# Performance work log

Measured on AMD Instinct MI355X. Metric: run time of the kernel, lower is better.

Reference implementation:

```python
import jax, jax.numpy as jnp
import numpy as np

T = 2048          # num tokens
HID = 2048        # hidden size
H = 16            # num heads
DN = 128          # qk_nope_head_dim
DR = 64           # qk_rope_head_dim
DV = 128          # v_head_dim
KV = 512          # kv_lora_rank
EPS = 1e-6
THETA = 10000.0
SCALE = (DN + DR) ** -0.5


def rmsnorm(x, w):
    var = jnp.mean(x * x, axis=-1, keepdims=True)
    return x * jax.lax.rsqrt(var + EPS) * w


def rope_interleaved(x, cos, sin):
    # x: [..., DR]; cos/sin broadcastable to [..., DR//2]; non-neox (interleaved pairs)
    x1 = x[..., 0::2]
    x2 = x[..., 1::2]
    o1 = x1 * cos - x2 * sin
    o2 = x2 * cos + x1 * sin
    return jnp.stack([o1, o2], axis=-1).reshape(x.shape)


def setup_inputs() -> dict:
    key = jax.random.key(0)
    ks = jax.random.split(key, 6)
    s = lambda fan_in: 1.0 / np.sqrt(fan_in)
    return {
        "positions": jnp.arange(T, dtype=jnp.int32),
        "hidden_states": jax.random.normal(ks[0], (T, HID), dtype=jnp.float32),
        "w_q": jax.random.normal(ks[1], (HID, H * (DN + DR)), dtype=jnp.float32) * s(HID),
        "w_kv_a": jax.random.normal(ks[2], (HID, KV + DR), dtype=jnp.float32) * s(HID),
        "kv_a_ln_w": jnp.ones((KV,), dtype=jnp.float32),
        "w_kv_b": jax.random.normal(ks[3], (KV, H * (DN + DV)), dtype=jnp.float32) * s(KV),
        "w_o": jax.random.normal(ks[4], (H * DV, HID), dtype=jnp.float32) * s(H * DV),
    }


def reference(positions, hidden_states, w_q, w_kv_a, kv_a_ln_w, w_kv_b, w_o):
    # Q projection (q_lora_rank is None -> direct q_proj)
    q = (hidden_states @ w_q).reshape(T, H, DN + DR)
    q_nope, q_pe = q[..., :DN], q[..., DN:]

    # KV latent + decoupled rope key
    kv = hidden_states @ w_kv_a              # [T, KV+DR]
    kv_c = rmsnorm(kv[:, :KV], kv_a_ln_w)    # [T, KV]
    k_pe = kv[:, KV:]                        # [T, DR]

    # RoPE (non-neox / interleaved)
    inv_freq = 1.0 / (THETA ** (jnp.arange(0, DR, 2, dtype=jnp.float32) / DR))
    freqs = positions.astype(jnp.float32)[:, None] * inv_freq   # [T, DR//2]
    cos, sin = jnp.cos(freqs), jnp.sin(freqs)
    q_pe = rope_interleaved(q_pe, cos[:, None, :], sin[:, None, :])  # [T, H, DR]
    k_pe = rope_interleaved(k_pe, cos, sin)                          # [T, DR]

    # Up-project latent to per-head K_nope / V
    kvb = (kv_c @ w_kv_b).reshape(T, H, DN + DV)
    k_nope, v = kvb[..., :DN], kvb[..., DN:]

    qf = jnp.concatenate([q_nope, q_pe], axis=-1)                    # [T, H, DN+DR]
    kf = jnp.concatenate([k_nope, jnp.broadcast_to(k_pe[:, None, :], (T, H, DR))], axis=-1)

    scores = jnp.einsum("qhd,khd->hqk", qf, kf) * SCALE              # [H, T, T]
    causal = jnp.tril(jnp.ones((T, T), dtype=bool))
    scores = jnp.where(causal, scores, jnp.finfo(scores.dtype).min)
    attn = jax.nn.softmax(scores, axis=-1)

    out = jnp.einsum("hqk,khd->qhd", attn, v).reshape(T, H * DV)
    return out @ w_o                                                 # [T, HID]
```

## Files before the change

kernel.cpp:

```cpp
#include <hip/hip_runtime.h>
#include <hip/hip_bf16.h>
#include <stdint.h>

#define T_N  2048
#define HID  2048
#define NH   16
#define DN   128
#define DR   64
#define DV   128
#define KVD  512
#define DQK  192
#define QDIM 3072
#define KVBD 4096
#define KVA  576
#define QKVN 3712
#define QBLK 128
#define KVBLK 64
#define TPH  40

typedef short  s16x8 __attribute__((ext_vector_type(8)));
typedef float  f32x4 __attribute__((ext_vector_type(4)));
typedef unsigned short u16;
typedef unsigned short u16x2 __attribute__((ext_vector_type(2)));
typedef unsigned short u16x4 __attribute__((ext_vector_type(4)));

#define NEG_INF (-__builtin_inff())
#define AS1 __attribute__((address_space(1)))
#define AS3 __attribute__((address_space(3)))
__device__ __constant__ float SCALE_C = 0.07216878364870323f;

__device__ __forceinline__ u16 f2b(float f) {
  unsigned u = __float_as_uint(f);
  u += 0x7fffu + ((u >> 16) & 1u);
  return (u16)(u >> 16);
}
__device__ __forceinline__ float b2f(u16 v) {
  return __uint_as_float(((unsigned)v) << 16);
}

__global__ void cast_and_tab(const float* __restrict__ x, u16* __restrict__ y,
                             const int* __restrict__ pos, float* __restrict__ ctab,
                             float* __restrict__ stab) {
  const int bid = blockIdx.x, tid = threadIdx.x;
  if (bid < 4096) {
    int i = bid * 256 + tid;
    float4 v = ((const float4*)x)[i];
    u16x4 o;
    o.x = f2b(v.x); o.y = f2b(v.y); o.z = f2b(v.z); o.w = f2b(v.w);
    ((u16x4*)y)[i] = o;
  } else {
    int i = (bid - 4096) * 256 + tid;
    int t = i >> 5, j = i & 31;
    float inv = powf(10000.f, -(float)(2 * j) / 64.f);
    float f = (float)pos[t] * inv;
    float s, c;
    sincosf(f, &s, &c);
    ctab[i] = c; stab[i] = s;
  }
}

#define TQK (QKVN / 32)
#define NB0 (TQK * (HID / 32))
#define NB1 ((KVBD / 32) * (KVD / 32))
#define NB2 ((HID / 32) * ((NH * DV) / 32))
__global__ void prep_weights(const float* __restrict__ wq, const float* __restrict__ wkva,
                             const float* __restrict__ wkvb, const float* __restrict__ wo,
                             u16* __restrict__ wqkvT, u16* __restrict__ wkvbT,
                             u16* __restrict__ woT)
{
  __shared__ float tile[32][33];
  int bid = blockIdx.x;
  const int tx = threadIdx.x, ty = threadIdx.y;
  int reg, n0, k0, K, N;
  const float* src = nullptr;
  u16* dst;
  if (bid < NB0)            { reg = 0; n0 = (bid % TQK) * 32;         k0 = (bid / TQK) * 32;         K = HID;     N = QKVN; dst = wqkvT; }
  else if (bid < NB0 + NB1) { bid -= NB0; reg = 1; n0 = (bid % (KVBD/32)) * 32; k0 = (bid / (KVBD/32)) * 32; K = KVD;  N = KVBD; src = wkvb; dst = wkvbT; }
  else                      { bid -= NB0 + NB1; reg = 2; n0 = (bid % (HID/32)) * 32; k0 = (bid / (HID/32)) * 32; K = NH*DV; N = HID; src = wo; dst = woT; }
#pragma unroll
  for (int i = 0; i < 4; ++i) {
    const int n = n0 + tx, k = k0 + ty + i * 8;
    float val;
    if (reg == 0) {
      if (n < QDIM) val = wq[(size_t)k * QDIM + n];
      else { int n2 = n - QDIM; val = (n2 < KVA) ? wkva[(size_t)k * KVA + n2] : 0.f; }
    } else {
      val = src[(size_t)k * N + n];
    }
    tile[ty + i * 8][tx] = val;
  }
  __syncthreads();
#pragma unroll
  for (int i = 0; i < 4; ++i)
    dst[(size_t)(n0 + ty + i * 8) * K + k0 + tx] = f2b(tile[tx][ty + i * 8]);
}

template <int MODE>
__global__ __launch_bounds__(256) void gemm_bf16(
    const u16* __restrict__ A, const u16* __restrict__ Bt,
    void* __restrict__ Cout, u16* __restrict__ vT, int M, int N, int K)
{
  __shared__ __align__(16) u16 As[8192];
  __shared__ __align__(16) u16 Bs[8192];
  const int tid  = threadIdx.x;
  const int lane = tid & 63;
  const int w    = tid >> 6;

  const int nwg = gridDim.x * gridDim.y;
  int id = blockIdx.y * gridDim.x + blockIdx.x;
  id = (id & 7) * (nwg >> 3) + (id >> 3);
  const int m0 = (id / gridDim.x) * 128, n0 = (id % gridDim.x) * 128;

  const int wm = (w >> 1) * 64, wn = (w & 1) * 64;

  const int r0   = tid >> 3;
  const int selE = (((tid & 7) ^ (r0 & 7)) << 3);
  const u16* sA = A  + (size_t)(m0 + r0) * K + selE;
  const u16* sB = Bt + (size_t)(n0 + r0) * K + selE;
  const int ldsOff = tid * 8;

  f32x4 acc[4][4];
  const f32x4 zero = {0.f, 0.f, 0.f, 0.f};
#pragma unroll
  for (int m = 0; m < 4; ++m)
#pragma unroll
    for (int n = 0; n < 4; ++n) acc[m][n] = zero;

  const int arow = lane & 15;
  const int kb   = (lane >> 4) * 16;
  const int KT = K >> 6;

  for (int kt = 0; kt < KT; ++kt) {
    const int ko = kt << 6;
    __syncthreads();
#pragma unroll
    for (int j = 0; j < 4; ++j) {
      __builtin_amdgcn_global_load_lds((const AS1 unsigned*)(sA + ko + (size_t)j * 32 * K),
                                       (AS3 unsigned*)(&As[ldsOff + j * 2048]), 16, 0, 0);
      __builtin_amdgcn_global_load_lds((const AS1 unsigned*)(sB + ko + (size_t)j * 32 * K),
                                       (AS3 unsigned*)(&Bs[ldsOff + j * 2048]), 16, 0, 0);
    }
    __syncthreads();
#pragma unroll
    for (int kk = 0; kk < 2; ++kk) {
      s16x8 af[4], bfr[4];
#pragma unroll
      for (int m = 0; m < 4; ++m) {
        const int r = wm + m * 16 + arow;
        af[m] = *(const s16x8*)((const char*)As + r * 128 + ((kk * 64 + kb) ^ ((r & 7) << 4)));
      }
#pragma unroll
      for (int n = 0; n < 4; ++n) {
        const int r = wn + n * 16 + arow;
        bfr[n] = *(const s16x8*)((const char*)Bs + r * 128 + ((kk * 64 + kb) ^ ((r & 7) << 4)));
      }
#pragma unroll
      for (int m = 0; m < 4; ++m)
#pragma unroll
        for (int n = 0; n < 4; ++n)
          acc[m][n] = __builtin_amdgcn_mfma_f32_16x16x32_bf16(af[m], bfr[n], acc[m][n], 0, 0, 0);
    }
  }

  const int r0w = (lane >> 4) * 4;
  const int cc = lane & 15;
  if constexpr (MODE == 2) {
    const int h = n0 >> 8;
    const bool vhalf = (n0 >> 7) & 1;
    u16* kf = (u16*)Cout;
#pragma unroll
    for (int m = 0; m < 4; ++m)
#pragma unroll
      for (int n = 0; n < 4; ++n) {
        const int d = wn + n * 16 + cc;
        const int trow = m0 + wm + m * 16 + r0w;
        if (!vhalf) {
#pragma unroll
          for (int r = 0; r < 4; ++r)
            kf[(size_t)(trow + r) * QDIM + h * DQK + d] = f2b(acc[m][n][r]);
        } else {
          u16x4 o;
          o.x = f2b(acc[m][n][0]); o.y = f2b(acc[m][n][1]);
          o.z = f2b(acc[m][n][2]); o.w = f2b(acc[m][n][3]);
          *(u16x4*)&vT[((size_t)h * 128 + d) * T_N + trow] = o;
        }
      }
  } else {
#pragma unroll
    for (int m = 0; m < 4; ++m)
#pragma unroll
      for (int n = 0; n < 4; ++n)
#pragma unroll
        for (int r = 0; r < 4; ++r) {
          const size_t idx = (size_t)(m0 + wm + m * 16 + r0w + r) * N + (n0 + wn + n * 16 + cc);
          if constexpr (MODE == 1) ((u16*)Cout)[idx] = f2b(acc[m][n][r]);
          else                     ((float*)Cout)[idx] = acc[m][n][r];
        }
  }
}

__global__ __launch_bounds__(256) void post_qkva(
    const u16* __restrict__ qkv, const float* __restrict__ lnw,
    const float* __restrict__ ctab, const float* __restrict__ stab,
    u16* __restrict__ kvc, u16* __restrict__ kf, u16* __restrict__ qfo)
{
  const int t = blockIdx.x;
  const int tid = threadIdx.x;
  __shared__ float csh[32], ssh[32], wsum[4];
  __shared__ u16 kpesh[64];
  if (tid < 32) { csh[tid] = ctab[t * 32 + tid]; ssh[tid] = stab[t * 32 + tid]; }

  const u16* row = qkv + (size_t)t * QKVN + QDIM;
  u16x2 v2 = *(const u16x2*)(row + tid * 2);
  float vx = b2f(v2.x), vy = b2f(v2.y);
  float ss = vx * vx + vy * vy;
#pragma unroll
  for (int d = 1; d < 64; d <<= 1) ss += __shfl_xor(ss, d, 64);
  if ((tid & 63) == 0) wsum[tid >> 6] = ss;
  __syncthreads();
  float tot = wsum[0] + wsum[1] + wsum[2] + wsum[3];
  float rs = rsqrtf(tot * (1.f / 512.f) + 1e-6f);
  float2 wv = *(const float2*)(lnw + tid * 2);
  kvc[(size_t)t * 512 + tid * 2]     = f2b(vx * rs * wv.x);
  kvc[(size_t)t * 512 + tid * 2 + 1] = f2b(vy * rs * wv.y);
  if (tid < 32) {
    float x1 = b2f(row[512 + 2 * tid]), x2 = b2f(row[513 + 2 * tid]);
    kpesh[2 * tid]     = f2b(x1 * csh[tid] - x2 * ssh[tid]);
    kpesh[2 * tid + 1] = f2b(x2 * csh[tid] + x1 * ssh[tid]);
  }
  __syncthreads();
  {
    const int h = tid >> 4, d0 = (tid & 15) * 4;
    u16x4 kp = *(const u16x4*)&kpesh[d0];
    *(u16x4*)&kf[(size_t)t * QDIM + h * DQK + 128 + d0] = kp;
  }

  const float SC = SCALE_C;
#pragma unroll
  for (int i = 0; i < 6; ++i) {
    const int p = i * 256 + tid;
    const int h = p / 96, pr = p % 96;
    const u16* base = qkv + (size_t)t * QKVN + h * DQK;
    u16* ob = qfo + ((size_t)t * NH + h) * DQK;
    if (pr < 64) {
      int d = pr * 2;
      u16x2 v = *(const u16x2*)(base + d);
      ob[d]     = f2b(b2f(v.x) * SC);
      ob[d + 1] = f2b(b2f(v.y) * SC);
    } else {
      int j = pr - 64;
      u16x2 v = *(const u16x2*)(base + 128 + 2 * j);
      ob[128 + 2 * j]     = f2b((b2f(v.x) * csh[j] - b2f(v.y) * ssh[j]) * SC);
      ob[128 + 2 * j + 1] = f2b((b2f(v.y) * csh[j] + b2f(v.x) * ssh[j]) * SC);
    }
  }
}

__global__ __launch_bounds__(512) void attn_fwd(
    const u16* __restrict__ qf, const u16* __restrict__ kf,
    const u16* __restrict__ vT, u16* __restrict__ Opart,
    float* __restrict__ mpart, float* __restrict__ lpart)
{
  const int h = blockIdx.x;
  const int j = (TPH - 1) - blockIdx.y;
  int qt, c, S;
  if (j < 4)       { qt = j;                c = 0;        S = 1; }
  else if (j < 12) { int u = j-4;  qt = 4 + (u>>1);  c = u&1;     S = 2; }
  else if (j < 24) { int u = j-12; int q3 = u/3; qt = 8+q3; c = u-3*q3; S = 3; }
  else             { int u = j-24; qt = 12 + (u>>2); c = u&3;     S = 4; }
  const int n = 2 * qt + 2;
  const int kt0 = (c * n) / S, kt1 = ((c + 1) * n) / S;
  const int task = h * TPH + j;
  const int q0 = qt * QBLK;

  const int tid = threadIdx.x;
  const int w = tid >> 6, lane = tid & 63;
  const int qw = q0 + w * 16;
  const int l15 = lane & 15, lh = lane >> 4;
  const int qrow = qw + l15;

  __shared__ __align__(16) u16 Ks[KVBLK * 192];
  __shared__ __align__(16) u16 Vs[128 * 64];
  __shared__ __align__(16) u16 P[8][16][72];

  s16x8 aQ[6];
#pragma unroll
  for (int kg = 0; kg < 6; ++kg)
    aQ[kg] = *(const s16x8*)&qf[(size_t)qrow * QDIM + h * DQK + kg * 32 + lh * 8];

  f32x4 accO[8];
  const f32x4 zero = {0.f, 0.f, 0.f, 0.f};
#pragma unroll
  for (int vn = 0; vn < 8; ++vn) accO[vn] = zero;
  float mreg = NEG_INF, lreg = 0.f;

  const int rK = tid >> 3, cK = (tid & 7) * 16;
  const int rV = tid >> 2, cV = (tid & 3) * 16;
  const u16* gK = kf + (size_t)rK * QDIM + h * DQK;
  const u16* gV = vT + ((size_t)h * 128 + rV) * T_N;
  const int swK = (rK & 7) << 4;
  const int swV = (rV & 7) << 4;

  s16x8 stK[3], stV[2];
#pragma unroll
  for (int jj = 0; jj < 3; ++jj)
    stK[jj] = *(const s16x8*)((const char*)(gK + (size_t)(kt0 * KVBLK) * QDIM) + cK + jj * 128);
#pragma unroll
  for (int jj = 0; jj < 2; ++jj)
    stV[jj] = *(const s16x8*)((const char*)(gV + kt0 * KVBLK) + cV + jj * 64);

  for (int kt = kt0; kt < kt1; ++kt) {
    const int t0 = kt * KVBLK;
    __syncthreads();
#pragma unroll
    for (int jj = 0; jj < 3; ++jj)
      *(s16x8*)((char*)Ks + rK * 384 + ((cK + jj * 128) ^ swK)) = stK[jj];
#pragma unroll
    for (int jj = 0; jj < 2; ++jj)
      *(s16x8*)((char*)Vs + rV * 128 + ((cV + jj * 64) ^ swV)) = stV[jj];
    __syncthreads();
    if (kt + 1 < kt1) {
      const int tn = t0 + KVBLK;
#pragma unroll
      for (int jj = 0; jj < 3; ++jj)
        stK[jj] = *(const s16x8*)((const char*)(gK + (size_t)tn * QDIM) + cK + jj * 128);
#pragma unroll
      for (int jj = 0; jj < 2; ++jj)
        stV[jj] = *(const s16x8*)((const char*)(gV + tn) + cV + jj * 64);
    }

    f32x4 s[4];
#pragma unroll
    for (int ct = 0; ct < 4; ++ct) s[ct] = zero;
    const int swq = (l15 & 7) << 4;
    __builtin_amdgcn_s_setprio(1);
#pragma unroll
    for (int ct = 0; ct < 4; ++ct) {
      const char* kbase = (char*)Ks + (ct * 16 + l15) * 384;
#pragma unroll
      for (int kg = 0; kg < 6; ++kg) {
        s16x8 aK = *(const s16x8*)(kbase + ((kg * 64 + lh * 16) ^ swq));
        s[ct] = __builtin_amdgcn_mfma_f32_16x16x32_bf16(aK, aQ[kg], s[ct], 0, 0, 0);
      }
    }
    __builtin_amdgcn_s_setprio(0);

    const bool diag = (t0 + KVBLK > q0);
    if (diag) {
#pragma unroll
      for (int ct = 0; ct < 4; ++ct)
#pragma unroll
        for (int r = 0; r < 4; ++r)
          s[ct][r] = (t0 + ct * 16 + lh * 4 + r <= qrow) ? s[ct][r] : NEG_INF;
    }

    float mx = s[0][0];
#pragma unroll
    for (int ct = 0; ct < 4; ++ct)
#pragma unroll
      for (int r = 0; r < 4; ++r) mx = fmaxf(mx, s[ct][r]);
    mx = fmaxf(mx, __shfl_xor(mx, 16, 64));
    mx = fmaxf(mx, __shfl_xor(mx, 32, 64));
    if (mx > mreg + 8.f) {
      float sc = __expf(mreg - mx);
      lreg *= sc;
#pragma unroll
      for (int vn = 0; vn < 8; ++vn)
#pragma unroll
        for (int r = 0; r < 4; ++r) accO[vn][r] *= sc;
      mreg = mx;
    }
    float p[4][4];
    float ps = 0.f;
#pragma unroll
    for (int ct = 0; ct < 4; ++ct)
#pragma unroll
      for (int r = 0; r < 4; ++r) { p[ct][r] = __expf(s[ct][r] - mreg); ps += p[ct][r]; }
    ps += __shfl_xor(ps, 16, 64);
    ps += __shfl_xor(ps, 32, 64);
    lreg += ps;

#pragma unroll
    for (int ct = 0; ct < 4; ++ct) {
      u16x4 pk;
      pk.x = f2b(p[ct][0]); pk.y = f2b(p[ct][1]);
      pk.z = f2b(p[ct][2]); pk.w = f2b(p[ct][3]);
      *(u16x4*)&P[w][l15][ct * 16 + lh * 4] = pk;
    }
    asm volatile("s_waitcnt lgkmcnt(0)" ::: "memory");
    s16x8 pb0 = *(const s16x8*)&P[w][l15][lh * 8];
    s16x8 pb1 = *(const s16x8*)&P[w][l15][32 + lh * 8];

    __builtin_amdgcn_s_setprio(1);
#pragma unroll
    for (int vn = 0; vn < 8; ++vn) {
      const char* vbase = (char*)Vs + (vn * 16 + l15) * 128;
      s16x8 aV0 = *(const s16x8*)(vbase + ((lh * 16) ^ swq));
      s16x8 aV1 = *(const s16x8*)(vbase + ((64 + lh * 16) ^ swq));
      accO[vn] = __builtin_amdgcn_mfma_f32_16x16x32_bf16(aV0, pb0, accO[vn], 0, 0, 0);
      accO[vn] = __builtin_amdgcn_mfma_f32_16x16x32_bf16(aV1, pb1, accO[vn], 0, 0, 0);
    }
    __builtin_amdgcn_s_setprio(0);
  }

  u16* Ob = Opart + ((size_t)task << 14);
  const int rl = w * 16 + l15;
#pragma unroll
  for (int vn = 0; vn < 8; ++vn) {
    u16x4 o;
    o.x = f2b(accO[vn][0]); o.y = f2b(accO[vn][1]);
    o.z = f2b(accO[vn][2]); o.w = f2b(accO[vn][3]);
    *(u16x4*)&Ob[rl * 128 + vn * 16 + lh * 4] = o;
  }
  if (lane < 16) {
    mpart[task * 128 + rl] = mreg;
    lpart[task * 128 + rl] = lreg;
  }
}

__global__ __launch_bounds__(256) void attn_merge(
    const u16* __restrict__ Opart, const float* __restrict__ mpart,
    const float* __restrict__ lpart, u16* __restrict__ attno)
{
  const int h = blockIdx.x >> 4, qt = blockIdx.x & 15;
  const int S = (qt >> 2) + 1;
  int base;
  if (qt < 4) base = qt; else if (qt < 8) base = 4 + 2*(qt-4);
  else if (qt < 12) base = 12 + 3*(qt-8); else base = 24 + 4*(qt-12);
  const int task0 = h * TPH + base;
  const int tid = threadIdx.x;
  __shared__ float wn[4][128];
  if (tid < 128) {
    float mc[4], lc[4];
    float M = NEG_INF;
    for (int c = 0; c < S; ++c) {
      mc[c] = mpart[(task0 + c) * 128 + tid];
      lc[c] = lpart[(task0 + c) * 128 + tid];
      M = fmaxf(M, mc[c]);
    }
    float L = 0.f, e[4];
    for (int c = 0; c < S; ++c) { e[c] = __expf(mc[c] - M); L += lc[c] * e[c]; }
    float Li = 1.f / L;
    for (int c = 0; c < S; ++c) wn[c][tid] = e[c] * Li;
  }
  __syncthreads();
  const int q0 = qt * QBLK;
#pragma unroll 4
  for (int k = 0; k < 16; ++k) {
    int bidx = k * 1024 + tid * 4;
    int row = bidx >> 7, col = bidx & 127;
    float a0 = 0.f, a1 = 0.f, a2 = 0.f, a3 = 0.f;
    for (int c = 0; c < S; ++c) {
      u16x4 v = *(const u16x4*)&Opart[(((size_t)(task0 + c)) << 14) + bidx];
      float wgt = wn[c][row];
      a0 += wgt * b2f(v.x); a1 += wgt * b2f(v.y);
      a2 += wgt * b2f(v.z); a3 += wgt * b2f(v.w);
    }
    u16x4 o; o.x = f2b(a0); o.y = f2b(a1); o.z = f2b(a2); o.w = f2b(a3);
    *(u16x4*)&attno[(size_t)(q0 + row) * (NH * DV) + h * DV + col] = o;
  }
}

extern "C" void kernel_launch(void* const* d_in, const int* in_sizes, int n_in,
                              void* d_out, int out_size, void* d_ws, size_t ws_size,
                              hipStream_t stream)
{
  const int*   positions = (const int*)d_in[0];
  const float* hs    = (const float*)d_in[1];
  const float* w_q   = (const float*)d_in[2];
  const float* w_kva = (const float*)d_in[3];
  const float* lnw   = (const float*)d_in[4];
  const float* w_kvb = (const float*)d_in[5];
  const float* w_o   = (const float*)d_in[6];
  float* out = (float*)d_out;

  char* ws = (char*)d_ws;
  size_t off = 0;
  auto take = [&](size_t bytes) {
    char* p = ws + off;
    off += (bytes + 255) & ~(size_t)255;
    return p;
  };

  u16*   hsb  = (u16*)  take((size_t)T_N * HID * 2);
  u16*   woT  = (u16*)  take((size_t)HID * (NH * DV) * 2);
  u16*   qfb  = (u16*)  take((size_t)T_N * QDIM * 2);
  u16*   kfb  = (u16*)  take((size_t)T_N * QDIM * 2);
  u16*   vTb  = (u16*)  take((size_t)NH * 128 * T_N * 2);
  float* ctab = (float*)take((size_t)T_N * 32 * 4);
  float* stab = (float*)take((size_t)T_N * 32 * 4);

  size_t un0 = off;
  u16*   wqkvT = (u16*)  take((size_t)QKVN * HID * 2);
  u16*   wkvbT = (u16*)  take((size_t)KVBD * KVD * 2);
  u16*   kvc   = (u16*)  take((size_t)T_N * KVD * 2);
  u16*   qkvb  = (u16*)  take((size_t)T_N * KVBD * 2);
  u16*   Opart = (u16*)(ws + un0);
  float* mpart = (float*)(Opart + ((size_t)NH * TPH << 14));
  float* lpart = mpart + (size_t)NH * TPH * 128;
  u16*   attno = hsb;

  (void)positions; (void)in_sizes; (void)n_in; (void)out_size; (void)ws_size;

  cast_and_tab<<<dim3(4096 + 256), dim3(256), 0, stream>>>(hs, hsb, positions, ctab, stab);
  prep_weights<<<dim3(NB0 + NB1 + NB2), dim3(32, 8), 0, stream>>>(w_q, w_kva, w_kvb, w_o,
                                                                  wqkvT, wkvbT, woT);

  gemm_bf16<1><<<dim3(QKVN / 128, T_N / 128), dim3(256), 0, stream>>>(hsb, wqkvT, qkvb, nullptr, T_N, QKVN, HID);
  post_qkva<<<dim3(T_N), dim3(256), 0, stream>>>(qkvb, lnw, ctab, stab, kvc, kfb, qfb);

  gemm_bf16<2><<<dim3(KVBD / 128, T_N / 128), dim3(256), 0, stream>>>(kvc, wkvbT, kfb, vTb, T_N, KVBD, KVD);

  attn_fwd<<<dim3(NH, TPH), dim3(512), 0, stream>>>(qfb, kfb, vTb, Opart, mpart, lpart);
  attn_merge<<<dim3(NH * 16), dim3(256), 0, stream>>>(Opart, mpart, lpart, attno);

  gemm_bf16<0><<<dim3(HID / 128, T_N / 128), dim3(256), 0, stream>>>(attno, woT, out, nullptr, T_N, HID, HID);
}
```

Measured before the change: 208.3 us.

## Merge prep kernels and replace LDS P round-trip with ds_bpermute in attention

```diff
diff --git a/kernel.cpp b/kernel.cpp
--- a/kernel.cpp
+++ b/kernel.cpp
@@ -38,39 +38,42 @@
   return __uint_as_float(((unsigned)v) << 16);
 }
 
-__global__ void cast_and_tab(const float* __restrict__ x, u16* __restrict__ y,
-                             const int* __restrict__ pos, float* __restrict__ ctab,
-                             float* __restrict__ stab) {
-  const int bid = blockIdx.x, tid = threadIdx.x;
-  if (bid < 4096) {
+#define TQK (QKVN / 32)
+#define NBC 4096
+#define NBT 256
+#define NB0 (TQK * (HID / 32))
+#define NB1 ((KVBD / 32) * (KVD / 32))
+#define NB2 ((HID / 32) * ((NH * DV) / 32))
+__global__ __launch_bounds__(256) void prep_all(
+    const float* __restrict__ hs, u16* __restrict__ hsb,
+    const int* __restrict__ pos, float* __restrict__ ctab, float* __restrict__ stab,
+    const float* __restrict__ wq, const float* __restrict__ wkva,
+    const float* __restrict__ wkvb, const float* __restrict__ wo,
+    u16* __restrict__ wqkvT, u16* __restrict__ wkvbT, u16* __restrict__ woT)
+{
+  int bid = blockIdx.x;
+  const int tid = threadIdx.x;
+  if (bid < NBC) {
     int i = bid * 256 + tid;
-    float4 v = ((const float4*)x)[i];
+    float4 v = ((const float4*)hs)[i];
     u16x4 o;
     o.x = f2b(v.x); o.y = f2b(v.y); o.z = f2b(v.z); o.w = f2b(v.w);
-    ((u16x4*)y)[i] = o;
-  } else {
-    int i = (bid - 4096) * 256 + tid;
+    ((u16x4*)hsb)[i] = o;
+    return;
+  }
+  if (bid < NBC + NBT) {
+    int i = (bid - NBC) * 256 + tid;
     int t = i >> 5, j = i & 31;
     float inv = powf(10000.f, -(float)(2 * j) / 64.f);
     float f = (float)pos[t] * inv;
     float s, c;
     sincosf(f, &s, &c);
     ctab[i] = c; stab[i] = s;
-  }
-}
-
-#define TQK (QKVN / 32)
-#define NB0 (TQK * (HID / 32))
-#define NB1 ((KVBD / 32) * (KVD / 32))
-#define NB2 ((HID / 32) * ((NH * DV) / 32))
-__global__ void prep_weights(const float* __restrict__ wq, const float* __restrict__ wkva,
-                             const float* __restrict__ wkvb, const float* __restrict__ wo,
-                             u16* __restrict__ wqkvT, u16* __restrict__ wkvbT,
-                             u16* __restrict__ woT)
-{
+    return;
+  }
+  bid -= NBC + NBT;
   __shared__ float tile[32][33];
-  int bid = blockIdx.x;
-  const int tx = threadIdx.x, ty = threadIdx.y;
+  const int tx = tid & 31, ty = tid >> 5;
   int reg, n0, k0, K, N;
   const float* src = nullptr;
   u16* dst;
@@ -256,7 +259,7 @@
   }
 }
 
-__global__ __launch_bounds__(512) void attn_fwd(
+__global__ __launch_bounds__(512, 6) void attn_fwd(
     const u16* __restrict__ qf, const u16* __restrict__ kf,
     const u16* __restrict__ vT, u16* __restrict__ Opart,
     float* __restrict__ mpart, float* __restrict__ lpart)
@@ -278,10 +281,10 @@
   const int qw = q0 + w * 16;
   const int l15 = lane & 15, lh = lane >> 4;
   const int qrow = qw + l15;
+  (void)w;
 
   __shared__ __align__(16) u16 Ks[KVBLK * 192];
   __shared__ __align__(16) u16 Vs[128 * 64];
-  __shared__ __align__(16) u16 P[8][16][72];
 
   s16x8 aQ[6];
 #pragma unroll
@@ -309,6 +312,10 @@
   for (int jj = 0; jj < 2; ++jj)
     stV[jj] = *(const s16x8*)((const char*)(gV + kt0 * KVBLK) + cV + jj * 64);
 
+  const int a0 = (l15 + ((lh & 1) << 5)) << 2;
+  const int a1 = a0 + 64;
+  const bool hi = (lh & 2) != 0;
+
   for (int kt = kt0; kt < kt1; ++kt) {
     const int t0 = kt * KVBLK;
     __syncthreads();
@@ -380,16 +387,45 @@
     ps += __shfl_xor(ps, 32, 64);
     lreg += ps;
 
-#pragma unroll
-    for (int ct = 0; ct < 4; ++ct) {
-      u16x4 pk;
-      pk.x = f2b(p[ct][0]); pk.y = f2b(p[ct][1]);
-      pk.z = f2b(p[ct][2]); pk.w = f2b(p[ct][3]);
-      *(u16x4*)&P[w][l15][ct * 16 + lh * 4] = pk;
-    }
-    asm volatile("s_waitcnt lgkmcnt(0)" ::: "memory");
-    s16x8 pb0 = *(const s16x8*)&P[w][l15][lh * 8];
-    s16x8 pb1 = *(const s16x8*)&P[w][l15][32 + lh * 8];
+    unsigned pk00 = (unsigned)f2b(p[0][0]) | ((unsigned)f2b(p[0][1]) << 16);
+    unsigned pk01 = (unsigned)f2b(p[0][2]) | ((unsigned)f2b(p[0][3]) << 16);
+    unsigned pk10 = (unsigned)f2b(p[1][0]) | ((unsigned)f2b(p[1][1]) << 16);
+    unsigned pk11 = (unsigned)f2b(p[1][2]) | ((unsigned)f2b(p[1][3]) << 16);
+    unsigned pk20 = (unsigned)f2b(p[2][0]) | ((unsigned)f2b(p[2][1]) << 16);
+    unsigned pk21 = (unsigned)f2b(p[2][2]) | ((unsigned)f2b(p[2][3]) << 16);
+    unsigned pk30 = (unsigned)f2b(p[3][0]) | ((unsigned)f2b(p[3][1]) << 16);
+    unsigned pk31 = (unsigned)f2b(p[3][2]) | ((unsigned)f2b(p[3][3]) << 16);
+
+    union { unsigned u[4]; s16x8 v; } U0, U1;
+    {
+      unsigned ta, tb;
+      ta = (unsigned)__builtin_amdgcn_ds_bpermute(a0, (int)pk00);
+      tb = (unsigned)__builtin_amdgcn_ds_bpermute(a0, (int)pk10);
+      U0.u[0] = hi ? tb : ta;
+      ta = (unsigned)__builtin_amdgcn_ds_bpermute(a0, (int)pk01);
+      tb = (unsigned)__builtin_amdgcn_ds_bpermute(a0, (int)pk11);
+      U0.u[1] = hi ? tb : ta;
+      ta = (unsigned)__builtin_amdgcn_ds_bpermute(a1, (int)pk00);
+      tb = (unsigned)__builtin_amdgcn_ds_bpermute(a1, (int)pk10);
+      U0.u[2] = hi ? tb : ta;
+      ta = (unsigned)__builtin_amdgcn_ds_bpermute(a1, (int)pk01);
+      tb = (unsigned)__builtin_amdgcn_ds_bpermute(a1, (int)pk11);
+      U0.u[3] = hi ? tb : ta;
+      ta = (unsigned)__builtin_amdgcn_ds_bpermute(a0, (int)pk20);
+      tb = (unsigned)__builtin_amdgcn_ds_bpermute(a0, (int)pk30);
+      U1.u[0] = hi ? tb : ta;
+      ta = (unsigned)__builtin_amdgcn_ds_bpermute(a0, (int)pk21);
+      tb = (unsigned)__builtin_amdgcn_ds_bpermute(a0, (int)pk31);
+      U1.u[1] = hi ? tb : ta;
+      ta = (unsigned)__builtin_amdgcn_ds_bpermute(a1, (int)pk20);
+      tb = (unsigned)__builtin_amdgcn_ds_bpermute(a1, (int)pk30);
+      U1.u[2] = hi ? tb : ta;
+      ta = (unsigned)__builtin_amdgcn_ds_bpermute(a1, (int)pk21);
+      tb = (unsigned)__builtin_amdgcn_ds_bpermute(a1, (int)pk31);
+      U1.u[3] = hi ? tb : ta;
+    }
+    s16x8 pb0 = U0.v;
+    s16x8 pb1 = U1.v;
 
     __builtin_amdgcn_s_setprio(1);
 #pragma unroll
@@ -404,7 +440,7 @@
   }
 
   u16* Ob = Opart + ((size_t)task << 14);
-  const int rl = w * 16 + l15;
+  const int rl = (tid >> 6) * 16 + l15;
 #pragma unroll
   for (int vn = 0; vn < 8; ++vn) {
     u16x4 o;
@@ -502,9 +538,8 @@
 
   (void)positions; (void)in_sizes; (void)n_in; (void)out_size; (void)ws_size;
 
-  cast_and_tab<<<dim3(4096 + 256), dim3(256), 0, stream>>>(hs, hsb, positions, ctab, stab);
-  prep_weights<<<dim3(NB0 + NB1 + NB2), dim3(32, 8), 0, stream>>>(w_q, w_kva, w_kvb, w_o,
-                                                                  wqkvT, wkvbT, woT);
+  prep_all<<<dim3(NBC + NBT + NB0 + NB1 + NB2), dim3(256), 0, stream>>>(
+      hs, hsb, positions, ctab, stab, w_q, w_kva, w_kvb, w_o, wqkvT, wkvbT, woT);
 
   gemm_bf16<1><<<dim3(QKVN / 128, T_N / 128), dim3(256), 0, stream>>>(hsb, wqkvT, qkvb, nullptr, T_N, QKVN, HID);
   post_qkva<<<dim3(T_N), dim3(256), 0, stream>>>(qkvb, lnw, ctab, stab, kvc, kfb, qfb);
```

New measurement: 323.1 us. 1.55x slower.
